# Optimization experiments

Measured on AMD Instinct MI355X. Metric: run time of the kernel, lower is better.

The kernel has to match this reference:

```python
import jax, jax.numpy as jnp
import numpy as np

D = 1024      # d_model
H = 16        # heads
KD = 64       # per-head dim
STRIDE = 64   # local chunk size
LH = 8        # local heads
GH = H - LH   # global heads
C = 4         # attended positions per global head per chunk


def setup_inputs() -> dict:
    key = jax.random.key(0)
    ks = jax.random.split(key, 12)
    B, S = 4, 4096
    sc = 1.0 / np.sqrt(D)
    x = jax.random.normal(ks[0], (B, S, D), jnp.float32)
    input_mask = jax.random.randint(ks[1], (B, S), 0, 2).astype(bool)
    Wq = jax.random.normal(ks[2], (D, D), jnp.float32) * sc
    bq = jax.random.normal(ks[3], (D,), jnp.float32) * 0.01
    Wk = jax.random.normal(ks[4], (D, D), jnp.float32) * sc
    bk = jax.random.normal(ks[5], (D,), jnp.float32) * 0.01
    Wv = jax.random.normal(ks[6], (D, D), jnp.float32) * sc
    bv = jax.random.normal(ks[7], (D,), jnp.float32) * 0.01
    Wo = jax.random.normal(ks[8], (D, D), jnp.float32) * sc
    bo = jax.random.normal(ks[9], (D,), jnp.float32) * 0.01
    return {"x": x, "input_mask": input_mask, "Wq": Wq, "bq": bq,
            "Wk": Wk, "bk": bk, "Wv": Wv, "bv": bv, "Wo": Wo, "bo": bo}


def reference(x, input_mask, Wq, bq, Wk, bk, Wv, bv, Wo, bo):
    B, S, _ = x.shape
    q = (x @ Wq.T + bq).reshape(B, S, H, KD)
    k = (x @ Wk.T + bk).reshape(B, S, H, KD)
    v = (x @ Wv.T + bv).reshape(B, S, H, KD)

    # ---- local heads: per the original code, the local attention scores are
    # computed but discarded; local_qkv = chunk_local_value reshaped back,
    # which is exactly the (head-major) local values. We reproduce that math.
    local_qkv = jnp.transpose(v[:, :, :LH, :], (0, 2, 1, 3))  # (B, LH, S, KD)

    # ---- global heads: each global head attends, inside every chunk, to a
    # fixed window of C positions near the end of the chunk.
    nc = S // STRIDE
    start = STRIDE - GH * C
    base = jnp.arange(start, STRIDE).reshape(GH, C)          # (GH, C)
    offs = jnp.arange(0, S, STRIDE)                          # (nc,)
    idx = (base[:, None, :] + offs[None, :, None]).reshape(GH, nc * C)  # (GH, L)
    L = nc * C

    gq = jnp.transpose(q[:, :, LH:, :], (0, 2, 1, 3))        # (B, GH, S, KD)
    gk = jnp.transpose(k[:, :, LH:, :], (0, 2, 1, 3))
    gv = jnp.transpose(v[:, :, LH:, :], (0, 2, 1, 3))

    h_idx = jnp.arange(GH)[:, None]                          # (GH, 1)
    gk_sel = gk[:, h_idx, idx, :]                            # (B, GH, L, KD)
    gv_sel = gv[:, h_idx, idx, :]                            # (B, GH, L, KD)

    qk = jnp.einsum('bhsd,bhld->bhsl', gq, gk_sel) * (KD ** -0.5)
    gmask = input_mask[:, idx]                               # (B, GH, L)
    qk = jnp.where(gmask[:, :, None, :], jnp.float32(-1e10), qk)
    attn = jax.nn.softmax(qk, axis=-1)
    g_out = jnp.einsum('bhsl,bhld->bhsd', attn, gv_sel)      # (B, GH, S, KD)

    qkv = jnp.concatenate([local_qkv, g_out], axis=1)        # (B, H, S, KD)
    qkv = jnp.transpose(qkv, (0, 2, 1, 3)).reshape(B, S, H * KD)
    return qkv @ Wo.T + bo
```

## Files before the change

### kernel.cpp

```cpp
#include <hip/hip_runtime.h>
#include <stdint.h>


typedef __bf16 bf16_t;
typedef __bf16 bf16x4 __attribute__((ext_vector_type(4)));
typedef __bf16 bf16x8 __attribute__((ext_vector_type(8)));
typedef float floatx4 __attribute__((ext_vector_type(4)));

#define MFMA16(a, b, c) __builtin_amdgcn_mfma_f32_16x16x32_bf16((a), (b), (c), 0, 0, 0)

__device__ __forceinline__ void glds16(const bf16_t* g, const bf16_t* lds_base) {
  __builtin_amdgcn_global_load_lds(
      (const __attribute__((address_space(1))) uint32_t*)(uintptr_t)g,
      (__attribute__((address_space(3))) uint32_t*)(uintptr_t)lds_base, 16, 0, 0);
}

#define VMCNT(n)  asm volatile("s_waitcnt vmcnt(" #n ")" ::: "memory")
#define LGKMCNT0  asm volatile("s_waitcnt lgkmcnt(0)" ::: "memory")
#define SBAR      __builtin_amdgcn_s_barrier()
#define SCHED0    __builtin_amdgcn_sched_barrier(0)

__global__ void cvt_f32_bf16(const float* __restrict__ src, bf16_t* __restrict__ dst, int n) {
  const int i = (blockIdx.x * 256 + threadIdx.x) * 4;
  if (i < n) {
    float4 v = *(const float4*)(src + i);
    bf16x4 d = {(bf16_t)v.x, (bf16_t)v.y, (bf16_t)v.z, (bf16_t)v.w};
    *(bf16x4*)(dst + i) = d;
  }
}

__global__ void pack_bias(const float* __restrict__ bv, const float* __restrict__ bq,
                          const float* __restrict__ bk, float* __restrict__ bcat) {
  const int i = blockIdx.x * 256 + threadIdx.x;
  float v;
  if (i < 1024) v = bv[i];
  else if (i < 1536) v = bq[i - 512];
  else v = bk[i - 1024];
  bcat[i] = v;
}

#define G8_DECL                                                                 \
  __shared__ bf16_t As[2][16384];                                               \
  __shared__ bf16_t Bs[2][16384];                                               \
  const int tid = threadIdx.x;                                                  \
  const int w = tid >> 6, l = tid & 63;                                         \
  const int lq = l >> 4, lm = l & 15;                                           \
  const int wr = (w >> 2) << 7;                      \
  const int wc = (w & 3) << 6;                \
  floatx4 acc[8][4];                                                            \
  { floatx4 z = {0.f, 0.f, 0.f, 0.f};                                           \
    _Pragma("unroll") for (int i = 0; i < 8; ++i)                               \
    _Pragma("unroll") for (int j = 0; j < 4; ++j) acc[i][j] = z; }              \
  const int t7 = tid & 127, t8 = tid >> 7;                                      \
  const int sbase = ((((w >> 1) << 8) + ((w & 1) << 6)) << 3);

#define G8_ST_A(s, off, jk)                                                     \
  glds16(pAt + (off),         &As[s][0] + ((jk) << 13) + sbase);                \
  glds16(pAt + aoff2 + (off), &As[s][0] + ((jk) << 13) + 1024 + sbase);
#define G8_ST_B(s, off, jk)                                                     \
  glds16(pBt + (off),          &Bs[s][0] + ((jk) << 13) + sbase);               \
  glds16(pBt + 131072 + (off), &Bs[s][0] + ((jk) << 13) + 1024 + sbase);

#define G8_READ_B(s, kk)                                                        \
  _Pragma("unroll") for (int nt = 0; nt < 4; ++nt)                              \
    bfr[nt] = *(const bf16x8*)(&Bs[s][0] +                                      \
        (((((kk) * 4 + lq) << 8) + wc + nt * 16 + lm) << 3));

#define G8_READ_A(s, kk, mh)                                                    \
  _Pragma("unroll") for (int i = 0; i < 4; ++i)                                 \
    af[i] = *(const bf16x8*)(&As[s][0] +                                        \
        (((((kk) * 4 + lq) << 8) + wr + (mh) * 64 + i * 16 + lm) << 3));

#define G8_MFMA(mh)                                                             \
  __builtin_amdgcn_s_setprio(1);                                                \
  _Pragma("unroll") for (int i = 0; i < 4; ++i)                                 \
    _Pragma("unroll") for (int nt = 0; nt < 4; ++nt)                            \
      acc[(mh) * 4 + i][nt] = MFMA16(af[i], bfr[nt], acc[(mh) * 4 + i][nt]);    \
  __builtin_amdgcn_s_setprio(0);

#define PH_PRE   SCHED0; SBAR; LGKMCNT0; SCHED0;
#define PH_POST  SCHED0; SBAR; SCHED0;

#define G8_ITER                                                                 \
    G8_READ_A(0, 0, 0) G8_READ_B(0, 0)                                          \
    G8_ST_A(1, 96, 1)                                                           \
    PH_PRE G8_MFMA(0) PH_POST                                                   \
    G8_READ_A(0, 0, 1)                                                          \
    G8_ST_B(1, 96, 1)                                                           \
    VMCNT(4);                                                                   \
    PH_PRE G8_MFMA(1) PH_POST                                                   \
    G8_READ_A(0, 1, 0) G8_READ_B(0, 1)                                          \
    G8_ST_A(0, 128, 0)                                                          \
    PH_PRE G8_MFMA(0) PH_POST                                                   \
    G8_READ_A(0, 1, 1)                                                          \
    G8_ST_B(0, 128, 0)                                                          \
    PH_PRE G8_MFMA(1) PH_POST                                                   \
    G8_READ_A(1, 0, 0) G8_READ_B(1, 0)                                          \
    G8_ST_A(0, 160, 1)                                                          \
    PH_PRE G8_MFMA(0) PH_POST                                                   \
    G8_READ_A(1, 0, 1)                                                          \
    G8_ST_B(0, 160, 1)                                                          \
    VMCNT(8);                                                                   \
    PH_PRE G8_MFMA(1) PH_POST                                                   \
    G8_READ_A(1, 1, 0) G8_READ_B(1, 1)                                          \
    G8_ST_A(1, 192, 0)                                                          \
    PH_PRE G8_MFMA(0) PH_POST                                                   \
    G8_READ_A(1, 1, 1)                                                          \
    G8_ST_B(1, 192, 0)                                                          \
    VMCNT(8);                                                                   \
    PH_PRE G8_MFMA(1) PH_POST

#define G8_TAIL                                                                 \
    G8_READ_A(0, 0, 0) G8_READ_B(0, 0)                                          \
    G8_ST_A(1, 96, 1)                                                           \
    PH_PRE G8_MFMA(0) PH_POST                                                   \
    G8_READ_A(0, 0, 1)                                                          \
    G8_ST_B(1, 96, 1)                                                           \
    VMCNT(4);                                                                   \
    PH_PRE G8_MFMA(1) PH_POST                                                   \
    G8_READ_A(0, 1, 0) G8_READ_B(0, 1)                                          \
    PH_PRE G8_MFMA(0) PH_POST                                                   \
    G8_READ_A(0, 1, 1)                                                          \
    PH_PRE G8_MFMA(1) PH_POST                                                   \
    G8_READ_A(1, 0, 0) G8_READ_B(1, 0)                                          \
    PH_PRE G8_MFMA(0) PH_POST                                                   \
    G8_READ_A(1, 0, 1)                                                          \
    VMCNT(0);                                                                   \
    PH_PRE G8_MFMA(1) PH_POST                                                   \
    G8_READ_A(1, 1, 0) G8_READ_B(1, 1)                                          \
    PH_PRE G8_MFMA(0) PH_POST                                                   \
    G8_READ_A(1, 1, 1)                                                          \
    PH_PRE G8_MFMA(1) PH_POST

#define G8_MAIN                                                                 \
  G8_ST_A(0, 0, 0) G8_ST_B(0, 0, 0)                                             \
  G8_ST_A(0, 32, 1) G8_ST_B(0, 32, 1)                                           \
  G8_ST_A(1, 64, 0) G8_ST_B(1, 64, 0)                                           \
  VMCNT(0); SBAR; SCHED0;                                                       \
  bf16x8 af[4], bfr[4];                                                         \
  for (int t = 0; t < 7; ++t) {                                                 \
    G8_ITER                                                                     \
    pAt += 128; pBt += 128;                                                     \
  }                                                                             \
  G8_TAIL

__global__ __launch_bounds__(512, 2)
void gemm_fused(const bf16_t* __restrict__ A, const bf16_t* __restrict__ Wcat,
                const float* __restrict__ bcat, bf16_t* __restrict__ qkv,
                bf16_t* __restrict__ vg, bf16_t* __restrict__ qg,
                bf16_t* __restrict__ kg) {
  G8_DECL
  const int n = blockIdx.x;
  long row0, col0;
  int aoff2;
  const bf16_t* pAt;
  if (n < 256) {
    const int xcd = n & 7, j = n >> 3;
    const int ct = j >> 3;
    row0 = (long)(xcd * 8 + (j & 7)) * 256;
    col0 = ct * 256 + (ct >= 2 ? 512 : 0);
    aoff2 = 131072;
    pAt = A + (row0 + t7) * 1024 + t8 * 8;
  } else {
    const int m2 = n - 256;
    const int xcd = m2 & 7, j = m2 >> 3;
    const int ct = j >> 2;
    row0 = (long)(xcd * 4 + (j & 3)) * 256;
    col0 = (ct < 2) ? (512 + ct * 256) : (1536 + (ct - 2) * 256);
    aoff2 = 262144;
    long r = row0 + t7;
    if (r > 8063) r = 8063;
    const long g = ((r >> 5) << 6) + 32 + (r & 31);
    pAt = A + g * 1024 + t8 * 8;
  }
  const bf16_t* pBt = Wcat + (col0 + t7) * 1024 + t8 * 8;
  G8_MAIN
  bf16_t* dst; long ld, cofs;
  if (col0 < 512)       { dst = qkv; ld = 1024; cofs = 0; }
  else if (col0 < 1024) { dst = vg;  ld = 512;  cofs = 512; }
  else if (col0 < 1536) { dst = qg;  ld = 512;  cofs = 1024; }
  else                  { dst = kg;  ld = 512;  cofs = 1536; }
#pragma unroll
  for (int nt = 0; nt < 4; ++nt) {
    const long col = col0 + wc + nt * 16 + lm;
    const float bc = bcat[col];
    const long cl = col - cofs;
#pragma unroll
    for (int mt = 0; mt < 8; ++mt) {
#pragma unroll
      for (int r = 0; r < 4; ++r) {
        const long row = row0 + wr + mt * 16 + lq * 4 + r;
        dst[row * ld + cl] = (bf16_t)(acc[mt][nt][r] + bc);
      }
    }
  }
}

__global__ __launch_bounds__(512, 2)
void gemm_bt(const bf16_t* __restrict__ A, const bf16_t* __restrict__ W,
             const float* __restrict__ bias, float* __restrict__ C, int ldc) {
  G8_DECL
  const int n = blockIdx.x, xcd = n & 7, j = n >> 3;
  const long row0 = (long)(xcd * 8 + (j & 7)) * 256;
  const long col0 = (long)(j >> 3) * 256;
  const int aoff2 = 131072;
  const bf16_t* pAt = A + (row0 + t7) * 1024 + t8 * 8;
  const bf16_t* pBt = W + (col0 + t7) * 1024 + t8 * 8;
  G8_MAIN
#pragma unroll
  for (int nt = 0; nt < 4; ++nt) {
    const long col = col0 + wc + nt * 16 + lm;
    const float bc = bias[col];
#pragma unroll
    for (int mt = 0; mt < 8; ++mt) {
#pragma unroll
      for (int r = 0; r < 4; ++r) {
        const long row = row0 + wr + mt * 16 + lq * 4 + r;
        C[row * (long)ldc + col] = acc[mt][nt][r] + bc;
      }
    }
  }
}

__global__ __launch_bounds__(512, 1)
void attn_sparse(const bf16_t* __restrict__ qg, const bf16_t* __restrict__ kg,
                 const bf16_t* __restrict__ vg, const int* __restrict__ mask,
                 bf16_t* __restrict__ qkv) {
  __shared__ bf16_t Ks[16384];
  __shared__ bf16_t Vt[64 * 264];
  __shared__ bf16_t Ps[8 * 16 * 136];
  __shared__ int smask[256];

  const int tid = threadIdx.x;
  const int b = blockIdx.z, h = blockIdx.y, qq = blockIdx.x;

  {
    const int lk = tid & 255;
    const int hf = tid >> 8;
    const int selrow = ((lk >> 2) << 5) + (h << 2) + (lk & 3);
    const size_t rowi = (size_t)(b * 2048 + selrow);
    const uint4* ksrc = (const uint4*)(kg + rowi * 512 + h * 64);
#pragma unroll
    for (int kq = 0; kq < 4; ++kq) {
      const int kq8 = hf * 4 + kq;
      *(uint4*)(Ks + (kq8 * 256 + lk) * 8) = ksrc[kq8];
    }
    const bf16_t* vsrc = vg + rowi * 512 + h * 64;
#pragma unroll
    for (int i = 0; i < 4; ++i) {
      const int i8 = hf * 4 + i;
      bf16x8 vv = *(const bf16x8*)(vsrc + i8 * 8);
#pragma unroll
      for (int j = 0; j < 8; ++j) Vt[(i8 * 8 + j) * 264 + lk] = vv[j];
    }
    if (tid < 256) {
      const int token = ((lk >> 2) << 6) + 32 + (h << 2) + (lk & 3);
      smask[lk] = mask[b * 4096 + token];
    }
  }
  __syncthreads();

  const int w = tid >> 6, l = tid & 63, lq = l >> 4, lm = l & 15;
  bf16_t* Pw = Ps + w * (16 * 136);
  floatx4 zero4 = {0.f, 0.f, 0.f, 0.f};

  for (int p = 0; p < 4; ++p) {
    const int mrow = (qq << 9) + ((p * 8 + w) << 4);

    const bf16_t* qrow = qg + (size_t)(b * 4096 + mrow + lm) * 512 + h * 64 + lq * 8;
    bf16x8 aq0 = *(const bf16x8*)qrow;
    bf16x8 aq1 = *(const bf16x8*)(qrow + 32);

    floatx4 s[16];
#pragma unroll
    for (int t = 0; t < 16; ++t) {
      bf16x8 kb0 = *(const bf16x8*)(Ks + (lq * 256 + t * 16 + lm) * 8);
      bf16x8 kb1 = *(const bf16x8*)(Ks + ((4 + lq) * 256 + t * 16 + lm) * 8);
      floatx4 z = zero4;
      z = MFMA16(aq0, kb0, z);
      z = MFMA16(aq1, kb1, z);
      s[t] = z;
    }

    float rmax[4] = {-1e30f, -1e30f, -1e30f, -1e30f};
#pragma unroll
    for (int t = 0; t < 16; ++t) {
      const bool mk = smask[t * 16 + lm] != 0;
#pragma unroll
      for (int r = 0; r < 4; ++r) {
        float v = s[t][r] * 0.125f;
        v = mk ? -1e10f : v;
        s[t][r] = v;
        rmax[r] = fmaxf(rmax[r], v);
      }
    }
#pragma unroll
    for (int off = 1; off < 16; off <<= 1)
#pragma unroll
      for (int r = 0; r < 4; ++r) rmax[r] = fmaxf(rmax[r], __shfl_xor(rmax[r], off));
    float rsum[4] = {0.f, 0.f, 0.f, 0.f};
#pragma unroll
    for (int t = 0; t < 16; ++t)
#pragma unroll
      for (int r = 0; r < 4; ++r) {
        float pp = __expf(s[t][r] - rmax[r]);
        s[t][r] = pp;
        rsum[r] += pp;
      }
#pragma unroll
    for (int off = 1; off < 16; off <<= 1)
#pragma unroll
      for (int r = 0; r < 4; ++r) rsum[r] += __shfl_xor(rsum[r], off);
    float rinv[4];
#pragma unroll
    for (int r = 0; r < 4; ++r) rinv[r] = 1.0f / rsum[r];

    floatx4 o[4];
#pragma unroll
    for (int dt = 0; dt < 4; ++dt) o[dt] = zero4;
#pragma unroll
    for (int half = 0; half < 2; ++half) {
#pragma unroll
      for (int t = 0; t < 8; ++t) {
        const int tt = half * 8 + t;
#pragma unroll
        for (int r = 0; r < 4; ++r)
          Pw[(lq * 4 + r) * 136 + t * 16 + lm] = (bf16_t)(s[tt][r] * rinv[r]);
      }
#pragma unroll
      for (int ks = 0; ks < 4; ++ks) {
        bf16x8 pa = *(const bf16x8*)(Pw + lm * 136 + ks * 32 + lq * 8);
#pragma unroll
        for (int dt = 0; dt < 4; ++dt) {
          bf16x8 vb = *(const bf16x8*)(Vt + (dt * 16 + lm) * 264 + half * 128 + ks * 32 + lq * 8);
          o[dt] = MFMA16(pa, vb, o[dt]);
        }
      }
    }

#pragma unroll
    for (int dt = 0; dt < 4; ++dt) {
      const int d = dt * 16 + lm;
#pragma unroll
      for (int r = 0; r < 4; ++r) {
        const int token = mrow + lq * 4 + r;
        qkv[(size_t)(b * 4096 + token) * 1024 + 512 + h * 64 + d] = (bf16_t)o[dt][r];
      }
    }
  }
}

extern "C" void kernel_launch(void* const* d_in, const int* in_sizes, int n_in,
                              void* d_out, int out_size, void* d_ws, size_t ws_size,
                              hipStream_t stream) {
  const float* x   = (const float*)d_in[0];
  const int* mask  = (const int*)d_in[1];
  const float* Wq  = (const float*)d_in[2];
  const float* bq  = (const float*)d_in[3];
  const float* Wk  = (const float*)d_in[4];
  const float* bk  = (const float*)d_in[5];
  const float* Wv  = (const float*)d_in[6];
  const float* bv  = (const float*)d_in[7];
  const float* Wo  = (const float*)d_in[8];
  const float* bo  = (const float*)d_in[9];
  float* out = (float*)d_out;

  char* ws = (char*)d_ws;
  bf16_t* xb   = (bf16_t*)(ws);
  bf16_t* Wcat = (bf16_t*)(ws + 33554432L);
  bf16_t* Wob  = (bf16_t*)(ws + 37748736L);
  float*  bcat = (float*)(ws + 39845888L);
  bf16_t* vg   = (bf16_t*)(ws + 39854080L);
  bf16_t* qg   = (bf16_t*)(ws + 56631296L);
  bf16_t* kg   = (bf16_t*)(ws + 73408512L);
  bf16_t* qkv  = (bf16_t*)(ws + 90185728L);

  dim3 blk(256);
  cvt_f32_bf16<<<16384, blk, 0, stream>>>(x, xb, 16777216);
  cvt_f32_bf16<<<1024, blk, 0, stream>>>(Wv, Wcat, 1048576);
  cvt_f32_bf16<<<512, blk, 0, stream>>>(Wq + 524288, Wcat + 1048576, 524288);
  cvt_f32_bf16<<<512, blk, 0, stream>>>(Wk + 524288, Wcat + 1572864, 524288);
  cvt_f32_bf16<<<1024, blk, 0, stream>>>(Wo, Wob, 1048576);
  pack_bias<<<8, blk, 0, stream>>>(bv, bq, bk, bcat);

  gemm_fused<<<384, dim3(512), 0, stream>>>(xb, Wcat, bcat, qkv, vg, qg, kg);
  attn_sparse<<<dim3(8, 8, 4), dim3(512), 0, stream>>>(qg, kg, vg, mask, qkv);
  gemm_bt<<<256, dim3(512), 0, stream>>>(qkv, Wob, bo, out, 1024);
}
```

Baseline: 320.8 us.

## Fuse conversion kernels and fold gathered GEMM tiles into main GEMM blocks

Merges the five f32-to-bf16 conversion launches and the bias pack into one prep kernel to cut launch overhead. The fused QKV GEMM now launches 256 blocks instead of 384. Each block first computes its full 256x256 tile, then a second pass over a 256x128 half-tile covering the gathered-row V/K work. That second pass uses a narrower B tile and its own pipelined main loop. This balances work across one wave of blocks on the 256-CU device and removes the tail wave, at the cost of longer per-block runtime and more code.

```diff
diff --git a/kernel.cpp b/kernel.cpp
--- a/kernel.cpp
+++ b/kernel.cpp
@@ -20,23 +20,35 @@
 #define SBAR      __builtin_amdgcn_s_barrier()
 #define SCHED0    __builtin_amdgcn_sched_barrier(0)
 
-__global__ void cvt_f32_bf16(const float* __restrict__ src, bf16_t* __restrict__ dst, int n) {
-  const int i = (blockIdx.x * 256 + threadIdx.x) * 4;
-  if (i < n) {
-    float4 v = *(const float4*)(src + i);
-    bf16x4 d = {(bf16_t)v.x, (bf16_t)v.y, (bf16_t)v.z, (bf16_t)v.w};
-    *(bf16x4*)(dst + i) = d;
-  }
-}
-
-__global__ void pack_bias(const float* __restrict__ bv, const float* __restrict__ bq,
-                          const float* __restrict__ bk, float* __restrict__ bcat) {
-  const int i = blockIdx.x * 256 + threadIdx.x;
-  float v;
-  if (i < 1024) v = bv[i];
-  else if (i < 1536) v = bq[i - 512];
-  else v = bk[i - 1024];
-  bcat[i] = v;
+__global__ void prep(const float* __restrict__ x, const float* __restrict__ Wv,
+                     const float* __restrict__ Wq, const float* __restrict__ Wk,
+                     const float* __restrict__ Wo, const float* __restrict__ bv,
+                     const float* __restrict__ bq, const float* __restrict__ bk,
+                     bf16_t* __restrict__ xb, bf16_t* __restrict__ Wcat,
+                     bf16_t* __restrict__ Wob, float* __restrict__ bcat) {
+  const int blk = blockIdx.x, tid = threadIdx.x;
+  const float* src; bf16_t* dst; int i;
+  if (blk < 16384)      { src = x;           dst = xb;             i = (blk * 256 + tid) * 4; }
+  else if (blk < 17408) { src = Wv;          dst = Wcat;           i = ((blk - 16384) * 256 + tid) * 4; }
+  else if (blk < 17920) { src = Wq + 524288; dst = Wcat + 1048576; i = ((blk - 17408) * 256 + tid) * 4; }
+  else if (blk < 18432) { src = Wk + 524288; dst = Wcat + 1572864; i = ((blk - 17920) * 256 + tid) * 4; }
+  else if (blk < 19456) { src = Wo;          dst = Wob;            i = ((blk - 18432) * 256 + tid) * 4; }
+  else {
+    const int j = tid * 8;
+#pragma unroll
+    for (int k = 0; k < 8; ++k) {
+      const int idx = j + k;
+      float v;
+      if (idx < 1024) v = bv[idx];
+      else if (idx < 1536) v = bq[idx - 512];
+      else v = bk[idx - 1024];
+      bcat[idx] = v;
+    }
+    return;
+  }
+  float4 v = *(const float4*)(src + i);
+  bf16x4 d = {(bf16_t)v.x, (bf16_t)v.y, (bf16_t)v.z, (bf16_t)v.w};
+  *(bf16x4*)(dst + i) = d;
 }
 
 #define G8_DECL                                                                 \
@@ -144,6 +156,83 @@
   }                                                                             \
   G8_TAIL
 
+#define G2_ST_B(s, off, jk)                                                     \
+  glds16(pBt + (off), &Bs[s][0] + ((jk) << 12) + ((w) << 9));
+
+#define G2_READ_B(s, kk)                                                        \
+  _Pragma("unroll") for (int nt = 0; nt < 2; ++nt)                              \
+    bfr[nt] = *(const bf16x8*)(&Bs[s][0] +                                      \
+        (((((kk) * 4 + lq) << 7) + wc2 + nt * 16 + lm) << 3));
+
+#define G2_MFMA(mh)                                                             \
+  __builtin_amdgcn_s_setprio(1);                                                \
+  _Pragma("unroll") for (int i = 0; i < 4; ++i)                                 \
+    _Pragma("unroll") for (int nt = 0; nt < 2; ++nt)                            \
+      acc[(mh) * 4 + i][nt] = MFMA16(af[i], bfr[nt], acc[(mh) * 4 + i][nt]);    \
+  __builtin_amdgcn_s_setprio(0);
+
+#define G2_ITER                                                                 \
+    G8_READ_A(0, 0, 0) G2_READ_B(0, 0)                                          \
+    G8_ST_A(1, 96, 1)                                                           \
+    PH_PRE G2_MFMA(0) PH_POST                                                   \
+    G8_READ_A(0, 0, 1)                                                          \
+    G2_ST_B(1, 96, 1)                                                           \
+    VMCNT(3);                                                                   \
+    PH_PRE G2_MFMA(1) PH_POST                                                   \
+    G8_READ_A(0, 1, 0) G2_READ_B(0, 1)                                          \
+    G8_ST_A(0, 128, 0)                                                          \
+    PH_PRE G2_MFMA(0) PH_POST                                                   \
+    G8_READ_A(0, 1, 1)                                                          \
+    G2_ST_B(0, 128, 0)                                                          \
+    PH_PRE G2_MFMA(1) PH_POST                                                   \
+    G8_READ_A(1, 0, 0) G2_READ_B(1, 0)                                          \
+    G8_ST_A(0, 160, 1)                                                          \
+    PH_PRE G2_MFMA(0) PH_POST                                                   \
+    G8_READ_A(1, 0, 1)                                                          \
+    G2_ST_B(0, 160, 1)                                                          \
+    VMCNT(6);                                                                   \
+    PH_PRE G2_MFMA(1) PH_POST                                                   \
+    G8_READ_A(1, 1, 0) G2_READ_B(1, 1)                                          \
+    G8_ST_A(1, 192, 0)                                                          \
+    PH_PRE G2_MFMA(0) PH_POST                                                   \
+    G8_READ_A(1, 1, 1)                                                          \
+    G2_ST_B(1, 192, 0)                                                          \
+    VMCNT(6);                                                                   \
+    PH_PRE G2_MFMA(1) PH_POST
+
+#define G2_TAIL                                                                 \
+    G8_READ_A(0, 0, 0) G2_READ_B(0, 0)                                          \
+    G8_ST_A(1, 96, 1)                                                           \
+    PH_PRE G2_MFMA(0) PH_POST                                                   \
+    G8_READ_A(0, 0, 1)                                                          \
+    G2_ST_B(1, 96, 1)                                                           \
+    VMCNT(3);                                                                   \
+    PH_PRE G2_MFMA(1) PH_POST                                                   \
+    G8_READ_A(0, 1, 0) G2_READ_B(0, 1)                                          \
+    PH_PRE G2_MFMA(0) PH_POST                                                   \
+    G8_READ_A(0, 1, 1)                                                          \
+    PH_PRE G2_MFMA(1) PH_POST                                                   \
+    G8_READ_A(1, 0, 0) G2_READ_B(1, 0)                                          \
+    PH_PRE G2_MFMA(0) PH_POST                                                   \
+    G8_READ_A(1, 0, 1)                                                          \
+    VMCNT(0);                                                                   \
+    PH_PRE G2_MFMA(1) PH_POST                                                   \
+    G8_READ_A(1, 1, 0) G2_READ_B(1, 1)                                          \
+    PH_PRE G2_MFMA(0) PH_POST                                                   \
+    G8_READ_A(1, 1, 1)                                                          \
+    PH_PRE G2_MFMA(1) PH_POST
+
+#define G2_MAIN                                                                 \
+  G8_ST_A(0, 0, 0) G2_ST_B(0, 0, 0)                                             \
+  G8_ST_A(0, 32, 1) G2_ST_B(0, 32, 1)                                           \
+  G8_ST_A(1, 64, 0) G2_ST_B(1, 64, 0)                                           \
+  VMCNT(0); SBAR; SCHED0;                                                       \
+  for (int t = 0; t < 7; ++t) {                                                 \
+    G2_ITER                                                                     \
+    pAt += 128; pBt += 128;                                                     \
+  }                                                                             \
+  G2_TAIL
+
 __global__ __launch_bounds__(512, 2)
 void gemm_fused(const bf16_t* __restrict__ A, const bf16_t* __restrict__ Wcat,
                 const float* __restrict__ bcat, bf16_t* __restrict__ qkv,
@@ -151,46 +240,65 @@
                 bf16_t* __restrict__ kg) {
   G8_DECL
   const int n = blockIdx.x;
-  long row0, col0;
-  int aoff2;
-  const bf16_t* pAt;
-  if (n < 256) {
-    const int xcd = n & 7, j = n >> 3;
-    const int ct = j >> 3;
-    row0 = (long)(xcd * 8 + (j & 7)) * 256;
-    col0 = ct * 256 + (ct >= 2 ? 512 : 0);
-    aoff2 = 131072;
-    pAt = A + (row0 + t7) * 1024 + t8 * 8;
-  } else {
-    const int m2 = n - 256;
-    const int xcd = m2 & 7, j = m2 >> 3;
-    const int ct = j >> 2;
-    row0 = (long)(xcd * 4 + (j & 3)) * 256;
-    col0 = (ct < 2) ? (512 + ct * 256) : (1536 + (ct - 2) * 256);
-    aoff2 = 262144;
-    long r = row0 + t7;
-    if (r > 8063) r = 8063;
-    const long g = ((r >> 5) << 6) + 32 + (r & 31);
-    pAt = A + g * 1024 + t8 * 8;
-  }
+  const int xcd = n & 7, j = n >> 3;
+  const int ct = j >> 3;
+  const long row0 = (long)(xcd * 8 + (j & 7)) * 256;
+  const long col0 = ct * 256 + (ct >= 2 ? 512 : 0);
+  int aoff2 = 131072;
+  const bf16_t* pAt = A + (row0 + t7) * 1024 + t8 * 8;
   const bf16_t* pBt = Wcat + (col0 + t7) * 1024 + t8 * 8;
   G8_MAIN
-  bf16_t* dst; long ld, cofs;
-  if (col0 < 512)       { dst = qkv; ld = 1024; cofs = 0; }
-  else if (col0 < 1024) { dst = vg;  ld = 512;  cofs = 512; }
-  else if (col0 < 1536) { dst = qg;  ld = 512;  cofs = 1024; }
-  else                  { dst = kg;  ld = 512;  cofs = 1536; }
-#pragma unroll
-  for (int nt = 0; nt < 4; ++nt) {
-    const long col = col0 + wc + nt * 16 + lm;
-    const float bc = bcat[col];
-    const long cl = col - cofs;
-#pragma unroll
-    for (int mt = 0; mt < 8; ++mt) {
-#pragma unroll
-      for (int r = 0; r < 4; ++r) {
-        const long row = row0 + wr + mt * 16 + lq * 4 + r;
-        dst[row * ld + cl] = (bf16_t)(acc[mt][nt][r] + bc);
+  {
+    bf16_t* dst; long ld, cofs;
+    if (col0 < 512) { dst = qkv; ld = 1024; cofs = 0; }
+    else            { dst = qg;  ld = 512;  cofs = 1024; }
+#pragma unroll
+    for (int nt = 0; nt < 4; ++nt) {
+      const long col = col0 + wc + nt * 16 + lm;
+      const float bc = bcat[col];
+      const long cl = col - cofs;
+#pragma unroll
+      for (int mt = 0; mt < 8; ++mt) {
+#pragma unroll
+        for (int r = 0; r < 4; ++r) {
+          const long row = row0 + wr + mt * 16 + lq * 4 + r;
+          dst[row * ld + cl] = (bf16_t)(acc[mt][nt][r] + bc);
+        }
+      }
+    }
+  }
+  const int wc2 = (w & 3) << 5;
+  const int rem = j >> 2;
+  const int ct2 = rem >> 1, nh = rem & 1;
+  const long row2 = (long)(xcd * 4 + (j & 3)) * 256;
+  const long col2 = ((ct2 < 2) ? (512 + ct2 * 256) : (1536 + (ct2 - 2) * 256)) + nh * 128;
+  long r2 = row2 + t7;
+  if (r2 > 8063) r2 = 8063;
+  const long g2 = ((r2 >> 5) << 6) + 32 + (r2 & 31);
+  pAt = A + g2 * 1024 + t8 * 8;
+  aoff2 = 262144;
+  pBt = Wcat + (col2 + t7) * 1024 + t8 * 8;
+  { floatx4 z = {0.f, 0.f, 0.f, 0.f};
+#pragma unroll
+    for (int i = 0; i < 8; ++i)
+#pragma unroll
+      for (int jz = 0; jz < 4; ++jz) acc[i][jz] = z; }
+  G2_MAIN
+  {
+    bf16_t* dst2 = (ct2 < 2) ? vg : kg;
+    const long cofs2 = (ct2 < 2) ? 512 : 1536;
+#pragma unroll
+    for (int nt = 0; nt < 2; ++nt) {
+      const long col = col2 + wc2 + nt * 16 + lm;
+      const float bc = bcat[col];
+      const long cl = col - cofs2;
+#pragma unroll
+      for (int mt = 0; mt < 8; ++mt) {
+#pragma unroll
+        for (int r = 0; r < 4; ++r) {
+          const long row = row2 + wr + mt * 16 + lq * 4 + r;
+          dst2[row * 512 + cl] = (bf16_t)(acc[mt][nt][r] + bc);
+        }
       }
     }
   }
@@ -375,15 +483,9 @@
   bf16_t* kg   = (bf16_t*)(ws + 73408512L);
   bf16_t* qkv  = (bf16_t*)(ws + 90185728L);
 
-  dim3 blk(256);
-  cvt_f32_bf16<<<16384, blk, 0, stream>>>(x, xb, 16777216);
-  cvt_f32_bf16<<<1024, blk, 0, stream>>>(Wv, Wcat, 1048576);
-  cvt_f32_bf16<<<512, blk, 0, stream>>>(Wq + 524288, Wcat + 1048576, 524288);
-  cvt_f32_bf16<<<512, blk, 0, stream>>>(Wk + 524288, Wcat + 1572864, 524288);
-  cvt_f32_bf16<<<1024, blk, 0, stream>>>(Wo, Wob, 1048576);
-  pack_bias<<<8, blk, 0, stream>>>(bv, bq, bk, bcat);
-
-  gemm_fused<<<384, dim3(512), 0, stream>>>(xb, Wcat, bcat, qkv, vg, qg, kg);
+  prep<<<19457, dim3(256), 0, stream>>>(x, Wv, Wq, Wk, Wo, bv, bq, bk,
+                                        xb, Wcat, Wob, bcat);
+  gemm_fused<<<256, dim3(512), 0, stream>>>(xb, Wcat, bcat, qkv, vg, qg, kg);
   attn_sparse<<<dim3(8, 8, 4), dim3(512), 0, stream>>>(qg, kg, vg, mask, qkv);
   gemm_bt<<<256, dim3(512), 0, stream>>>(qkv, Wob, bo, out, 1024);
 }
```

New measurement: 303.7 us. -5.3%, faster.
